# Optimization experiments

Hardware: AMD Instinct MI355X
Metric: run time of the kernel (lower is better)

The kernel has to match this reference:

```python
import jax, jax.numpy as jnp
import numpy as np

B, IN, E, NCLS = 1024, 784, 256, 10
BRAIN, ADIM, NJUMPS = 4, 3, 4
N = BRAIN ** ADIM  # 64 blocks
TAU = 1.0
_GKEY = jax.random.key(42)  # fixed key -> deterministic gumbel noise


def _gumbel_softmax_hard(key, logits):
    u = jax.random.uniform(key, logits.shape, minval=1e-6, maxval=1.0 - 1e-6)
    g = -jnp.log(-jnp.log(u))
    y = jax.nn.softmax((logits + g) / TAU, axis=-1)
    hard = jax.nn.one_hot(jnp.argmax(y, axis=-1), logits.shape[-1], dtype=y.dtype)
    return jax.lax.stop_gradient(hard - y) + y  # straight-through


def _next_address(state, key, at0_W1, at0_b1, at0_W2, at0_b2):
    # always uses block 0's address_transform (as in the original forward)
    h = jax.nn.relu(state @ at0_W1 + at0_b1)
    logits = (h @ at0_W2 + at0_b2).reshape(state.shape[0], ADIM, BRAIN)
    return _gumbel_softmax_hard(key, logits)  # (B, ADIM, BRAIN) one-hot


def _all_blocks(state, st_W1, st_b1, st_W2, st_b2):
    # state: (B,E); st_W*: (N,E,E) stored (in,out). Two batched GEMMs over all N blocks.
    h = jax.nn.relu(jnp.einsum('be,neh->bnh', state, st_W1) + st_b1[None])
    h = jax.nn.relu(jnp.einsum('bnh,nhg->bng', h, st_W2) + st_b2[None])
    norm = jnp.linalg.norm(state, axis=1, keepdims=True)  # (B,1), norm of INPUT state
    return h / (norm[:, :, None] + 1e-6)  # (B,N,E)


def _flatten_onehot(oh):
    # (B, ADIM, BRAIN) -> (B, BRAIN**ADIM) via iterated outer product
    b = oh.shape[0]
    fw = oh[:, 0, :]
    for d in range(1, oh.shape[1]):
        fw = (fw[:, :, None] * oh[:, d, None, :]).reshape(b, -1)
    return fw


def _forward(x, W_emb, b_emb, st_W1, st_b1, st_W2, st_b2,
             at0_W1, at0_b1, at0_W2, at0_b2, out_W1, out_b1, out_W2, out_b2):
    bsz = x.shape[0]
    state = x.reshape(bsz, -1) @ W_emb + b_emb
    initial_state = state
    current_address = _next_address(state, jax.random.fold_in(_GKEY, 0),
                                    at0_W1, at0_b1, at0_W2, at0_b2)
    exited = jnp.zeros((bsz,), dtype=bool)
    exit_states = jnp.zeros_like(state)
    exit_addresses = jnp.zeros_like(current_address)
    for i in range(NJUMPS):  # fixed small jump count; early-break replaced by masking (same math)
        active = ~exited
        bw = _flatten_onehot(current_address)                      # (B,N)
        allout = _all_blocks(state, st_W1, st_b1, st_W2, st_b2)    # (B,N,E)
        new_state = jnp.einsum('bn,bne->be', bw, allout)
        new_address = _next_address(new_state, jax.random.fold_in(_GKEY, i + 1),
                                    at0_W1, at0_b1, at0_W2, at0_b2)
        idx = jnp.argmax(new_address, axis=2)
        is_origin = jnp.all(idx == 0, axis=1) & active
        exit_states = jnp.where(is_origin[:, None], new_state, exit_states)
        exit_addresses = jnp.where(is_origin[:, None, None], new_address, exit_addresses)
        exited = exited | is_origin
        state = jnp.where(active[:, None], new_state, state)
        current_address = jnp.where(active[:, None, None], new_address, current_address)
    final_address = jnp.where(exited[:, None, None], exit_addresses, current_address)
    bw = _flatten_onehot(final_address)
    # original code computes block_out twice and keeps the one using `state` (bug-faithful)
    allout = _all_blocks(state, st_W1, st_b1, st_W2, st_b2)
    final_output = jnp.einsum('bn,bne->be', bw, allout) + initial_state
    h = jax.nn.relu(final_output @ out_W1 + out_b1)
    return h @ out_W2 + out_b2  # (B, NCLS)


def setup_inputs() -> dict:
    key = jax.random.key(0)
    ks = jax.random.split(key, 16)
    s = 0.02
    return {
        'x': jax.random.normal(ks[0], (B, IN), jnp.float32),
        'W_emb': jax.random.normal(ks[1], (IN, E), jnp.float32) * s,
        'b_emb': jnp.zeros((E,), jnp.float32),
        'st_W1': jax.random.normal(ks[2], (N, E, E), jnp.float32) * s,
        'st_b1': jnp.zeros((N, E), jnp.float32),
        'st_W2': jax.random.normal(ks[3], (N, E, E), jnp.float32) * s,
        'st_b2': jnp.zeros((N, E), jnp.float32),
        'at0_W1': jax.random.normal(ks[4], (E, E), jnp.float32) * s,
        'at0_b1': jnp.zeros((E,), jnp.float32),
        'at0_W2': jax.random.normal(ks[5], (E, ADIM * BRAIN), jnp.float32) * s,
        'at0_b2': jnp.zeros((ADIM * BRAIN,), jnp.float32),
        'out_W1': jax.random.normal(ks[6], (E, E), jnp.float32) * s,
        'out_b1': jnp.zeros((E,), jnp.float32),
        'out_W2': jax.random.normal(ks[7], (E, NCLS), jnp.float32) * s,
        'out_b2': jnp.zeros((NCLS,), jnp.float32),
    }


def reference(x, W_emb, b_emb, st_W1, st_b1, st_W2, st_b2,
              at0_W1, at0_b1, at0_W2, at0_b2, out_W1, out_b1, out_W2, out_b2):
    return _forward(x, W_emb, b_emb, st_W1, st_b1, st_W2, st_b2,
                    at0_W1, at0_b1, at0_W2, at0_b2, out_W1, out_b1, out_W2, out_b2)
```

## Files before the change

kernel.cpp:

```cpp
#include <hip/hip_runtime.h>
#include <stdint.h>


#define BATCH 1024
#define EDIM  256
#define INDIM 784
#define CH    4
#define GRID_B 304

__host__ __device__ inline uint32_t rotl32(uint32_t x, uint32_t d) {
  return (x << d) | (x >> (32u - d));
}
__host__ __device__ inline void threefry2x32(uint32_t k0, uint32_t k1,
                                             uint32_t x0, uint32_t x1,
                                             uint32_t* o0, uint32_t* o1) {
  uint32_t ks2 = k0 ^ k1 ^ 0x1BD11BDAu;
  x0 += k0; x1 += k1;
#define TF_R(a) { x0 += x1; x1 = rotl32(x1, a); x1 ^= x0; }
  TF_R(13) TF_R(15) TF_R(26) TF_R(6)   x0 += k1;  x1 += ks2 + 1u;
  TF_R(17) TF_R(29) TF_R(16) TF_R(24)  x0 += ks2; x1 += k0  + 2u;
  TF_R(13) TF_R(15) TF_R(26) TF_R(6)   x0 += k0;  x1 += k1  + 3u;
  TF_R(17) TF_R(29) TF_R(16) TF_R(24)  x0 += k1;  x1 += ks2 + 4u;
  TF_R(13) TF_R(15) TF_R(26) TF_R(6)   x0 += ks2; x1 += k0  + 5u;
#undef TF_R
  *o0 = x0; *o1 = x1;
}
__device__ inline uint32_t jax_bits12288(uint32_t k0, uint32_t k1, uint32_t L) {
  uint32_t o0, o1;
  if (L < 6144u) { threefry2x32(k0, k1, L, L + 6144u, &o0, &o1); return o0; }
  else           { threefry2x32(k0, k1, L - 6144u, L, &o0, &o1); return o1; }
}
__device__ inline float jax_uniform(uint32_t bits) {
  const float minv = 1e-6f;
  const float maxv = (float)(1.0 - 1e-06);
  const float span = maxv - minv;
  uint32_t fb = (bits >> 9) | 0x3f800000u;
  float f = __uint_as_float(fb) - 1.0f;
  float u = __fadd_rn(__fmul_rn(f, span), minv);
  return fmaxf(minv, u);
}
__device__ inline float gumbel_val(int s, int b, int c) {
  uint32_t fk0, fk1;
  threefry2x32(0u, 42u, 0u, (uint32_t)s, &fk0, &fk1);
  const uint32_t L = (uint32_t)(b * 12 + c);
  const float u = jax_uniform(jax_bits12288(fk0, fk1, L));
  return -logf(-logf(u));
}
__device__ inline int addr_argmax(const float* v) {
  int i0 = 0, i1 = 0, i2 = 0;
  { float b = v[0];
    for (int c = 1; c < 4; c++) { float x = v[c];     if (x > b) { b = x; i0 = c; } } }
  { float b = v[4];
    for (int c = 1; c < 4; c++) { float x = v[4 + c]; if (x > b) { b = x; i1 = c; } } }
  { float b = v[8];
    for (int c = 1; c < 4; c++) { float x = v[8 + c]; if (x > b) { b = x; i2 = c; } } }
  return i0 * 16 + i1 * 4 + i2;
}

#define GEMM_TILE(Wbase, XSarr, SROW, kb, KS, acc)                              \
  {                                                                             \
    const float* Wc = (Wbase) + (size_t)(kb) * EDIM + jc;                       \
    _Pragma("unroll 1")                                                         \
    for (int kk = 0; kk < (KS); kk += 4) {                                      \
      float wv[16];                                                             \
      _Pragma("unroll")                                                         \
      for (int q = 0; q < 4; q++) {                                             \
        _Pragma("unroll")                                                       \
        for (int cc = 0; cc < 4; cc++)                                          \
          wv[q * 4 + cc] = Wc[(size_t)(kk + q) * EDIM + cc * 64];               \
      }                                                                         \
      const int k = (kb) + kk;                                                  \
      const float4 r0 = *(const float4*)&(XSarr)[0 * (SROW) + k];               \
      const float4 r1 = *(const float4*)&(XSarr)[1 * (SROW) + k];               \
      const float4 r2 = *(const float4*)&(XSarr)[2 * (SROW) + k];               \
      const float4 r3 = *(const float4*)&(XSarr)[3 * (SROW) + k];               \
      _Pragma("unroll")                                                         \
      for (int cc = 0; cc < 4; cc++) {                                          \
        acc[0][cc] = fmaf(r0.x, wv[0 + cc], acc[0][cc]);                        \
        acc[0][cc] = fmaf(r0.y, wv[4 + cc], acc[0][cc]);                        \
        acc[0][cc] = fmaf(r0.z, wv[8 + cc], acc[0][cc]);                        \
        acc[0][cc] = fmaf(r0.w, wv[12 + cc], acc[0][cc]);                       \
        acc[1][cc] = fmaf(r1.x, wv[0 + cc], acc[1][cc]);                        \
        acc[1][cc] = fmaf(r1.y, wv[4 + cc], acc[1][cc]);                        \
        acc[1][cc] = fmaf(r1.z, wv[8 + cc], acc[1][cc]);                        \
        acc[1][cc] = fmaf(r1.w, wv[12 + cc], acc[1][cc]);                       \
        acc[2][cc] = fmaf(r2.x, wv[0 + cc], acc[2][cc]);                        \
        acc[2][cc] = fmaf(r2.y, wv[4 + cc], acc[2][cc]);                        \
        acc[2][cc] = fmaf(r2.z, wv[8 + cc], acc[2][cc]);                        \
        acc[2][cc] = fmaf(r2.w, wv[12 + cc], acc[2][cc]);                       \
        acc[3][cc] = fmaf(r3.x, wv[0 + cc], acc[3][cc]);                        \
        acc[3][cc] = fmaf(r3.y, wv[4 + cc], acc[3][cc]);                        \
        acc[3][cc] = fmaf(r3.z, wv[8 + cc], acc[3][cc]);                        \
        acc[3][cc] = fmaf(r3.w, wv[12 + cc], acc[3][cc]);                       \
      }                                                                         \
    }                                                                           \
  }

#define P_STORE(P, kg, jc, acc)                                                 \
  { _Pragma("unroll")                                                           \
    for (int cc = 0; cc < 4; cc++) {                                            \
      const int col = (jc) + cc * 64;                                           \
      *(float4*)&(P)[(((kg) * 256) + col) * 4] =                                \
        make_float4(acc[0][cc], acc[1][cc], acc[2][cc], acc[3][cc]);            \
    } }

#define GEMM_TILE_H(Wbase, Harr, kb, KS, acc)                                   \
  {                                                                             \
    const float* Wc = (Wbase) + (size_t)(kb) * EDIM + jc;                       \
    _Pragma("unroll 1")                                                         \
    for (int kk = 0; kk < (KS); kk += 4) {                                      \
      float wv[16];                                                             \
      _Pragma("unroll")                                                         \
      for (int q = 0; q < 4; q++) {                                             \
        _Pragma("unroll")                                                       \
        for (int cc = 0; cc < 4; cc++)                                          \
          wv[q * 4 + cc] = Wc[(size_t)(kk + q) * EDIM + cc * 64];               \
      }                                                                         \
      _Pragma("unroll")                                                         \
      for (int q = 0; q < 4; q++) {                                             \
        const float4 h = *(const float4*)&(Harr)[((kb) + kk + q) * 4];          \
        _Pragma("unroll")                                                       \
        for (int cc = 0; cc < 4; cc++) {                                        \
          acc[0][cc] = fmaf(h.x, wv[q * 4 + cc], acc[0][cc]);                   \
          acc[1][cc] = fmaf(h.y, wv[q * 4 + cc], acc[1][cc]);                   \
          acc[2][cc] = fmaf(h.z, wv[q * 4 + cc], acc[2][cc]);                   \
          acc[3][cc] = fmaf(h.w, wv[q * 4 + cc], acc[3][cc]);                   \
        }                                                                       \
      }                                                                         \
    }                                                                           \
  }

#define ADDR_TAIL(P, H, P2a, vals, ab1, aW2, ab2, astep, b0)                    \
  {                                                                             \
    { const int col = t;                                                        \
      float4 p0 = *(const float4*)&(P)[((0 * 256) + col) * 4];                  \
      float4 p1 = *(const float4*)&(P)[((1 * 256) + col) * 4];                  \
      float4 p2 = *(const float4*)&(P)[((2 * 256) + col) * 4];                  \
      float4 p3 = *(const float4*)&(P)[((3 * 256) + col) * 4];                  \
      const float bb = (ab1)[col];                                              \
      *(float4*)&(H)[col * 4] = make_float4(                                    \
        fmaxf(p0.x + p1.x + p2.x + p3.x + bb, 0.f),                             \
        fmaxf(p0.y + p1.y + p2.y + p3.y + bb, 0.f),                             \
        fmaxf(p0.z + p1.z + p2.z + p3.z + bb, 0.f),                             \
        fmaxf(p0.w + p1.w + p2.w + p3.w + bb, 0.f));                            \
    }                                                                           \
    __syncthreads();                                                            \
    { const int c = t & 15, ksl = t >> 4;                                       \
      float a2[4] = {0.f, 0.f, 0.f, 0.f};                                       \
      if (c < 12) {                                                             \
        const int k0 = ksl * 16;                                                \
        _Pragma("unroll 4")                                                     \
        for (int k = k0; k < k0 + 16; k++) {                                    \
          const float4 h = *(const float4*)&(H)[k * 4];                         \
          const float w = (aW2)[k * 12 + c];                                    \
          a2[0] = fmaf(h.x, w, a2[0]); a2[1] = fmaf(h.y, w, a2[1]);             \
          a2[2] = fmaf(h.z, w, a2[2]); a2[3] = fmaf(h.w, w, a2[3]);             \
        }                                                                       \
      }                                                                         \
      *(float4*)&(P2a)[(ksl * 16 + c) * 4] = make_float4(a2[0], a2[1], a2[2], a2[3]); \
    }                                                                           \
    __syncthreads();                                                            \
    if (t < 48) {                                                               \
      const int i = t / 12, c = t % 12;                                         \
      float s = 0.f;                                                            \
      _Pragma("unroll")                                                         \
      for (int w = 0; w < 16; w++) s += (P2a)[(w * 16 + c) * 4 + i];            \
      (vals)[i * 12 + c] = s + (ab2)[c] + gumbel_val((astep), (b0) + i, c);     \
    }                                                                           \
    __syncthreads();                                                            \
  }

__global__ __launch_bounds__(256, 4) void k_embed_a0(
    const float* __restrict__ x, const float* __restrict__ Wemb,
    const float* __restrict__ bemb,
    const float* __restrict__ aW1, const float* __restrict__ ab1,
    const float* __restrict__ aW2, const float* __restrict__ ab2,
    float* __restrict__ state, float* __restrict__ initial,
    int* __restrict__ nn_all) {
  __shared__ __align__(16) float XS[4 * INDIM];
  __shared__ __align__(16) float P[4 * 256 * 4];
  __shared__ __align__(16) float SS[4 * EDIM];
  __shared__ __align__(16) float H[EDIM * 4];
  __shared__ __align__(16) float P2a[16 * 16 * 4];
  __shared__ float vals[4 * 12];
  const int t = threadIdx.x, b0 = blockIdx.x * 4;
  const int jc = t & 63, kg = t >> 6;

  { const float4* src = (const float4*)(x + (size_t)b0 * INDIM);
    for (int p = t; p < INDIM; p += 256) ((float4*)XS)[p] = src[p];
  }
  __syncthreads();

  {
    const int kb = kg * 196;
    float acc[4][4] = {};
    GEMM_TILE(Wemb, XS, INDIM, kb, 196, acc);
    P_STORE(P, kg, jc, acc);
  }
  __syncthreads();
  {
    const int col = t;
    float4 p0 = *(const float4*)&P[((0 * 256) + col) * 4];
    float4 p1 = *(const float4*)&P[((1 * 256) + col) * 4];
    float4 p2 = *(const float4*)&P[((2 * 256) + col) * 4];
    float4 p3 = *(const float4*)&P[((3 * 256) + col) * 4];
    const float bb = bemb[col];
    float s0 = p0.x + p1.x + p2.x + p3.x + bb;
    float s1 = p0.y + p1.y + p2.y + p3.y + bb;
    float s2 = p0.z + p1.z + p2.z + p3.z + bb;
    float s3 = p0.w + p1.w + p2.w + p3.w + bb;
    SS[0 * EDIM + col] = s0; SS[1 * EDIM + col] = s1;
    SS[2 * EDIM + col] = s2; SS[3 * EDIM + col] = s3;
    state[(size_t)(b0 + 0) * EDIM + col] = s0; initial[(size_t)(b0 + 0) * EDIM + col] = s0;
    state[(size_t)(b0 + 1) * EDIM + col] = s1; initial[(size_t)(b0 + 1) * EDIM + col] = s1;
    state[(size_t)(b0 + 2) * EDIM + col] = s2; initial[(size_t)(b0 + 2) * EDIM + col] = s2;
    state[(size_t)(b0 + 3) * EDIM + col] = s3; initial[(size_t)(b0 + 3) * EDIM + col] = s3;
  }
  __syncthreads();

  {
    const int kb = kg * 64;
    float acc[4][4] = {};
    GEMM_TILE(aW1, SS, EDIM, kb, 64, acc);
    P_STORE(P, kg, jc, acc);
  }
  __syncthreads();
  ADDR_TAIL(P, H, P2a, vals, ab1, aW2, ab2, 0, b0);
  if (t < 4) nn_all[b0 + t] = addr_argmax(&vals[t * 12]);
}

__global__ __launch_bounds__(256, 4) void k_addr(
    const float* __restrict__ state,
    const float* __restrict__ aW1, const float* __restrict__ ab1,
    const float* __restrict__ aW2, const float* __restrict__ ab2,
    const int* __restrict__ nn_prev, int* __restrict__ nn_out, int step) {
  __shared__ __align__(16) float XS[4 * EDIM];
  __shared__ __align__(16) float P[4 * 256 * 4];
  __shared__ __align__(16) float H[EDIM * 4];
  __shared__ __align__(16) float P2a[16 * 16 * 4];
  __shared__ float vals[4 * 12];
  const int t = threadIdx.x, b0 = blockIdx.x * 4;
  const int jc = t & 63, kg = t >> 6;

  ((float4*)XS)[t] = ((const float4*)(state + (size_t)b0 * EDIM))[t];
  __syncthreads();

  { const int kb = kg * 64;
    float acc[4][4] = {};
    GEMM_TILE(aW1, XS, EDIM, kb, 64, acc);
    P_STORE(P, kg, jc, acc);
  }
  __syncthreads();
  ADDR_TAIL(P, H, P2a, vals, ab1, aW2, ab2, step, b0);
  if (t < 4) {
    const int b = b0 + t;
    int nxt;
    if (nn_prev[b] < 0) nxt = -1;
    else {
      const int nn = addr_argmax(&vals[t * 12]);
      nxt = (step < 4 && nn == 0) ? -1 : nn;
    }
    nn_out[b] = nxt;
  }
}

#define B_ROUTE(nnval_expr)                                                     \
  if (t < 64) hist[t] = 0;                                                      \
  if (t < 4) rowsl[t] = 0;                                                      \
  __syncthreads();                                                              \
  int myv[4]; bool fl[4];                                                       \
  _Pragma("unroll")                                                             \
  for (int p = 0; p < 4; p++) {                                                 \
    const int rr = p * 256 + t;                                                 \
    myv[p] = (nnval_expr);                                                      \
    if (myv[p] >= 0) atomicAdd(&hist[myv[p]], 1);                               \
  }                                                                             \
  __syncthreads();                                                              \
  if (t < 64) {                                                                 \
    const int cnt = hist[t];                                                    \
    const int nch = (cnt + CH - 1) / CH;                                        \
    int icnt = cnt, inch = nch;                                                 \
    _Pragma("unroll")                                                           \
    for (int d = 1; d < 64; d <<= 1) {                                          \
      int t1 = __shfl_up(icnt, d), t2 = __shfl_up(inch, d);                     \
      if (t >= d) { icnt += t1; inch += t2; }                                   \
    }                                                                           \
    const int ench = inch - nch;                                                \
    if (t == 63) meta[3] = inch;                                                \
    if (c >= ench && c < ench + nch) {                                          \
      meta[0] = t; meta[1] = c - ench;                                          \
      meta[2] = min(CH, cnt - (c - ench) * CH);                                 \
    }                                                                           \
  }                                                                             \
  __syncthreads();                                                              \
  if (c >= meta[3]) return;                                                     \
  const int n = meta[0], local = meta[1], m = meta[2];                          \
  {                                                                             \
    const int wid = t >> 6, lane = t & 63;                                      \
    unsigned long long bals[4];                                                 \
    _Pragma("unroll")                                                           \
    for (int p = 0; p < 4; p++) {                                               \
      fl[p] = (myv[p] == n);                                                    \
      bals[p] = __ballot(fl[p]);                                                \
      if (lane == 0) wcnt2[p * 4 + wid] = __popcll(bals[p]);                    \
    }                                                                           \
    __syncthreads();                                                            \
    if (t == 0) { int s = 0;                                                    \
      for (int e = 0; e < 16; e++) { wbase2[e] = s; s += wcnt2[e]; } }          \
    __syncthreads();                                                            \
    const int r0 = local * CH;                                                  \
    _Pragma("unroll")                                                           \
    for (int p = 0; p < 4; p++) {                                               \
      if (fl[p]) {                                                              \
        const int rank = wbase2[p * 4 + wid] +                                  \
          __popcll(bals[p] & ((1ull << lane) - 1ull));                          \
        if (rank >= r0 && rank < r0 + CH) rowsl[rank - r0] = p * 256 + t;       \
      }                                                                         \
    }                                                                           \
    __syncthreads();                                                            \
  }

__global__ __launch_bounds__(256, 4) void k_blocks(
    float* __restrict__ state,
    const float* __restrict__ W1, const float* __restrict__ b1,
    const float* __restrict__ W2, const float* __restrict__ b2,
    const int* __restrict__ nnj) {
  __shared__ __align__(16) float XS[4 * EDIM];
  __shared__ __align__(16) float P[4 * 256 * 4];
  __shared__ __align__(16) float H[EDIM * 4];
  __shared__ int hist[64], meta[4], rowsl[4];
  __shared__ int wcnt2[16], wbase2[16];
  __shared__ float denom[4];
  const int t = threadIdx.x;
  const int c = ((blockIdx.x & 7) * 38) + (blockIdx.x >> 3);
  const int jc = t & 63, kg = t >> 6;

  B_ROUTE(nnj[rr])

  {
    const int i = t >> 6, q = t & 63;
    const int row = rowsl[min(i, m - 1)] & 1023;
    const float4 v = *(const float4*)(state + (size_t)row * EDIM + q * 4);
    ((float4*)XS)[t] = v;
    float sq = v.x * v.x + v.y * v.y + v.z * v.z + v.w * v.w;
#pragma unroll
    for (int d = 32; d >= 1; d >>= 1) sq += __shfl_xor(sq, d);
    if (q == 0) denom[i] = sqrtf(sq) + 1e-6f;
  }
  __syncthreads();

  const float* W1n = W1 + (size_t)n * EDIM * EDIM;
  const float* W2n = W2 + (size_t)n * EDIM * EDIM;
  const int kb = kg * 64;
  { float acc[4][4] = {};
    GEMM_TILE(W1n, XS, EDIM, kb, 64, acc);
    P_STORE(P, kg, jc, acc);
  }
  __syncthreads();
  {
    const int col = t;
    float4 p0 = *(const float4*)&P[((0 * 256) + col) * 4];
    float4 p1 = *(const float4*)&P[((1 * 256) + col) * 4];
    float4 p2 = *(const float4*)&P[((2 * 256) + col) * 4];
    float4 p3 = *(const float4*)&P[((3 * 256) + col) * 4];
    const float bb = b1[(size_t)n * EDIM + col];
    *(float4*)&H[col * 4] = make_float4(
      fmaxf(p0.x + p1.x + p2.x + p3.x + bb, 0.f),
      fmaxf(p0.y + p1.y + p2.y + p3.y + bb, 0.f),
      fmaxf(p0.z + p1.z + p2.z + p3.z + bb, 0.f),
      fmaxf(p0.w + p1.w + p2.w + p3.w + bb, 0.f));
  }
  __syncthreads();
  { float acc[4][4] = {};
    GEMM_TILE_H(W2n, H, kb, 64, acc);
    P_STORE(P, kg, jc, acc);
  }
  __syncthreads();
  {
    const int col = t;
    float4 p0 = *(const float4*)&P[((0 * 256) + col) * 4];
    float4 p1 = *(const float4*)&P[((1 * 256) + col) * 4];
    float4 p2 = *(const float4*)&P[((2 * 256) + col) * 4];
    float4 p3 = *(const float4*)&P[((3 * 256) + col) * 4];
    const float bb = b2[(size_t)n * EDIM + col];
    float s[4] = { p0.x + p1.x + p2.x + p3.x + bb,
                   p0.y + p1.y + p2.y + p3.y + bb,
                   p0.z + p1.z + p2.z + p3.z + bb,
                   p0.w + p1.w + p2.w + p3.w + bb };
#pragma unroll
    for (int i = 0; i < 4; i++) {
      if (i < m) {
        const int row = rowsl[i] & 1023;
        state[(size_t)row * EDIM + col] = fmaxf(s[i], 0.f) / denom[i];
      }
    }
  }
}

__global__ __launch_bounds__(256, 4) void k_block_final(
    const float* __restrict__ state,
    const float* __restrict__ W1, const float* __restrict__ b1,
    const float* __restrict__ W2, const float* __restrict__ b2,
    const float* __restrict__ initial,
    const float* __restrict__ oW1, const float* __restrict__ ob1,
    const float* __restrict__ oW2, const float* __restrict__ ob2,
    const int* __restrict__ nn4, float* __restrict__ out) {
  __shared__ __align__(16) float XS[4 * EDIM];
  __shared__ __align__(16) float P[4 * 256 * 4];
  __shared__ __align__(16) float H[EDIM * 4];
  __shared__ __align__(16) float P2h[8 * 16 * 4];
  __shared__ int hist[64], meta[4], rowsl[4];
  __shared__ int wcnt2[16], wbase2[16];
  __shared__ float denom[4];
  const int t = threadIdx.x;
  const int c = ((blockIdx.x & 7) * 38) + (blockIdx.x >> 3);
  const int jc = t & 63, kg = t >> 6;

  B_ROUTE(max(nn4[rr], 0))

  { const int i = t >> 6, q = t & 63;
    const int row = rowsl[min(i, m - 1)] & 1023;
    const float4 v = *(const float4*)(state + (size_t)row * EDIM + q * 4);
    ((float4*)XS)[t] = v;
    float sq = v.x * v.x + v.y * v.y + v.z * v.z + v.w * v.w;
#pragma unroll
    for (int d = 32; d >= 1; d >>= 1) sq += __shfl_xor(sq, d);
    if (q == 0) denom[i] = sqrtf(sq) + 1e-6f;
  }
  __syncthreads();

  const float* W1n = W1 + (size_t)n * EDIM * EDIM;
  const float* W2n = W2 + (size_t)n * EDIM * EDIM;
  const int kb = kg * 64;
  { float acc[4][4] = {};
    GEMM_TILE(W1n, XS, EDIM, kb, 64, acc);
    P_STORE(P, kg, jc, acc);
  }
  __syncthreads();
  { const int col = t;
    float4 p0 = *(const float4*)&P[((0 * 256) + col) * 4];
    float4 p1 = *(const float4*)&P[((1 * 256) + col) * 4];
    float4 p2 = *(const float4*)&P[((2 * 256) + col) * 4];
    float4 p3 = *(const float4*)&P[((3 * 256) + col) * 4];
    const float bb = b1[(size_t)n * EDIM + col];
    *(float4*)&H[col * 4] = make_float4(
      fmaxf(p0.x + p1.x + p2.x + p3.x + bb, 0.f),
      fmaxf(p0.y + p1.y + p2.y + p3.y + bb, 0.f),
      fmaxf(p0.z + p1.z + p2.z + p3.z + bb, 0.f),
      fmaxf(p0.w + p1.w + p2.w + p3.w + bb, 0.f));
  }
  __syncthreads();
  { float acc[4][4] = {};
    GEMM_TILE_H(W2n, H, kb, 64, acc);
    P_STORE(P, kg, jc, acc);
  }
  __syncthreads();
  {
    const int col = t;
    float4 p0 = *(const float4*)&P[((0 * 256) + col) * 4];
    float4 p1 = *(const float4*)&P[((1 * 256) + col) * 4];
    float4 p2 = *(const float4*)&P[((2 * 256) + col) * 4];
    float4 p3 = *(const float4*)&P[((3 * 256) + col) * 4];
    const float bb = b2[(size_t)n * EDIM + col];
    float s[4] = { p0.x + p1.x + p2.x + p3.x + bb,
                   p0.y + p1.y + p2.y + p3.y + bb,
                   p0.z + p1.z + p2.z + p3.z + bb,
                   p0.w + p1.w + p2.w + p3.w + bb };
#pragma unroll
    for (int i = 0; i < 4; i++) {
      const int row = rowsl[i] & 1023;
      float v = fmaxf(s[i], 0.f) / denom[i];
      v += initial[(size_t)row * EDIM + col];
      XS[i * EDIM + col] = v;
    }
  }
  __syncthreads();

  { float acc[4][4] = {};
    GEMM_TILE(oW1, XS, EDIM, kb, 64, acc);
    P_STORE(P, kg, jc, acc);
  }
  __syncthreads();
  { const int col = t;
    float4 p0 = *(const float4*)&P[((0 * 256) + col) * 4];
    float4 p1 = *(const float4*)&P[((1 * 256) + col) * 4];
    float4 p2 = *(const float4*)&P[((2 * 256) + col) * 4];
    float4 p3 = *(const float4*)&P[((3 * 256) + col) * 4];
    const float bb = ob1[col];
    *(float4*)&H[col * 4] = make_float4(
      fmaxf(p0.x + p1.x + p2.x + p3.x + bb, 0.f),
      fmaxf(p0.y + p1.y + p2.y + p3.y + bb, 0.f),
      fmaxf(p0.z + p1.z + p2.z + p3.z + bb, 0.f),
      fmaxf(p0.w + p1.w + p2.w + p3.w + bb, 0.f));
  }
  __syncthreads();
  {
    if (t < 128) {
      const int cc = t & 15, ksl = t >> 4;
      float a2[4] = {0.f, 0.f, 0.f, 0.f};
      if (cc < 10) {
        const int k0 = ksl * 32;
#pragma unroll 4
        for (int k = k0; k < k0 + 32; k++) {
          const float4 h = *(const float4*)&H[k * 4];
          const float w = oW2[k * 10 + cc];
          a2[0] = fmaf(h.x, w, a2[0]); a2[1] = fmaf(h.y, w, a2[1]);
          a2[2] = fmaf(h.z, w, a2[2]); a2[3] = fmaf(h.w, w, a2[3]);
        }
      }
      *(float4*)&P2h[(ksl * 16 + cc) * 4] = make_float4(a2[0], a2[1], a2[2], a2[3]);
    }
  }
  __syncthreads();
  if (t < 40) {
    const int i = t / 10, cc = t % 10;
    if (i < m) {
      float s = 0.f;
#pragma unroll
      for (int w = 0; w < 8; w++) s += P2h[(w * 16 + cc) * 4 + i];
      const int row = rowsl[i] & 1023;
      out[(size_t)row * 10 + cc] = s + ob2[cc];
    }
  }
}

extern "C" void kernel_launch(void* const* d_in, const int* in_sizes, int n_in,
                              void* d_out, int out_size, void* d_ws, size_t ws_size,
                              hipStream_t stream) {
  const float* x    = (const float*)d_in[0];
  const float* Wemb = (const float*)d_in[1];
  const float* bemb = (const float*)d_in[2];
  const float* stW1 = (const float*)d_in[3];
  const float* stb1 = (const float*)d_in[4];
  const float* stW2 = (const float*)d_in[5];
  const float* stb2 = (const float*)d_in[6];
  const float* aW1  = (const float*)d_in[7];
  const float* ab1  = (const float*)d_in[8];
  const float* aW2  = (const float*)d_in[9];
  const float* ab2  = (const float*)d_in[10];
  const float* oW1  = (const float*)d_in[11];
  const float* ob1  = (const float*)d_in[12];
  const float* oW2  = (const float*)d_in[13];
  const float* ob2  = (const float*)d_in[14];
  float* out = (float*)d_out;

  char* ws = (char*)d_ws;
  auto alloc = [&](size_t bytes) { char* p = ws; ws += (bytes + 255) & ~(size_t)255; return p; };
  float* state   = (float*)alloc((size_t)BATCH * EDIM * 4);
  float* initial = (float*)alloc((size_t)BATCH * EDIM * 4);
  int*   nn_all  = (int*)alloc(5 * BATCH * 4);

  k_embed_a0<<<BATCH / 4, 256, 0, stream>>>(x, Wemb, bemb, aW1, ab1, aW2, ab2,
                                            state, initial, nn_all);
  for (int j = 0; j < 4; j++) {
    k_blocks<<<GRID_B, 256, 0, stream>>>(state, stW1, stb1, stW2, stb2,
                                         nn_all + j * BATCH);
    k_addr<<<BATCH / 4, 256, 0, stream>>>(state, aW1, ab1, aW2, ab2,
                                          nn_all + j * BATCH,
                                          nn_all + (j + 1) * BATCH, j + 1);
  }
  k_block_final<<<GRID_B, 256, 0, stream>>>(state, stW1, stb1, stW2, stb2,
                                            initial, oW1, ob1, oW2, ob2,
                                            nn_all + 4 * BATCH, out);
}
```

Baseline: 255.2 us.

## Double thread count per block with 8-way split-K and double-buffered weight loads

All kernels move from 256 to 512 threads, splitting the K dimension of each GEMM tile across 8 thread groups instead of 4, with an 8-way shared-memory partial-sum reduction. The GEMM inner loops now prefetch the next group of weight values into a second register buffer while the current one is used, to hide global load latency. The aim is more warps in flight per block for these latency-bound small GEMMs, at the cost of more shared memory, a longer reduction, and idle threads in the reduction phases.

```diff
diff --git a/kernel.cpp b/kernel.cpp
--- a/kernel.cpp
+++ b/kernel.cpp
@@ -57,100 +57,106 @@
   return i0 * 16 + i1 * 4 + i2;
 }
 
+#define LDW16(dst, Wc, kkq)                                                     \
+  { _Pragma("unroll")                                                           \
+    for (int _q = 0; _q < 4; _q++) {                                            \
+      _Pragma("unroll")                                                         \
+      for (int _cc = 0; _cc < 4; _cc++)                                         \
+        dst[_q * 4 + _cc] = (Wc)[(size_t)((kkq) + _q) * EDIM + _cc * 64];       \
+    } }
+
+#define FMA16(acc, wv, XSarr, SROW, kabs)                                       \
+  { const float4 _r0 = *(const float4*)&(XSarr)[0 * (SROW) + (kabs)];           \
+    const float4 _r1 = *(const float4*)&(XSarr)[1 * (SROW) + (kabs)];           \
+    const float4 _r2 = *(const float4*)&(XSarr)[2 * (SROW) + (kabs)];           \
+    const float4 _r3 = *(const float4*)&(XSarr)[3 * (SROW) + (kabs)];           \
+    _Pragma("unroll")                                                           \
+    for (int _cc = 0; _cc < 4; _cc++) {                                         \
+      acc[0][_cc] = fmaf(_r0.x, wv[0 + _cc], acc[0][_cc]);                      \
+      acc[0][_cc] = fmaf(_r0.y, wv[4 + _cc], acc[0][_cc]);                      \
+      acc[0][_cc] = fmaf(_r0.z, wv[8 + _cc], acc[0][_cc]);                      \
+      acc[0][_cc] = fmaf(_r0.w, wv[12 + _cc], acc[0][_cc]);                     \
+      acc[1][_cc] = fmaf(_r1.x, wv[0 + _cc], acc[1][_cc]);                      \
+      acc[1][_cc] = fmaf(_r1.y, wv[4 + _cc], acc[1][_cc]);                      \
+      acc[1][_cc] = fmaf(_r1.z, wv[8 + _cc], acc[1][_cc]);                      \
+      acc[1][_cc] = fmaf(_r1.w, wv[12 + _cc], acc[1][_cc]);                     \
+      acc[2][_cc] = fmaf(_r2.x, wv[0 + _cc], acc[2][_cc]);                      \
+      acc[2][_cc] = fmaf(_r2.y, wv[4 + _cc], acc[2][_cc]);                      \
+      acc[2][_cc] = fmaf(_r2.z, wv[8 + _cc], acc[2][_cc]);                      \
+      acc[2][_cc] = fmaf(_r2.w, wv[12 + _cc], acc[2][_cc]);                     \
+      acc[3][_cc] = fmaf(_r3.x, wv[0 + _cc], acc[3][_cc]);                      \
+      acc[3][_cc] = fmaf(_r3.y, wv[4 + _cc], acc[3][_cc]);                      \
+      acc[3][_cc] = fmaf(_r3.z, wv[8 + _cc], acc[3][_cc]);                      \
+      acc[3][_cc] = fmaf(_r3.w, wv[12 + _cc], acc[3][_cc]);                     \
+    } }
+
 #define GEMM_TILE(Wbase, XSarr, SROW, kb, KS, acc)                              \
-  {                                                                             \
-    const float* Wc = (Wbase) + (size_t)(kb) * EDIM + jc;                       \
+  { const float* _Wc = (Wbase) + (size_t)(kb) * EDIM + jc;                      \
+    float _wvA[16], _wvB[16];                                                   \
+    LDW16(_wvA, _Wc, 0)                                                         \
     _Pragma("unroll 1")                                                         \
-    for (int kk = 0; kk < (KS); kk += 4) {                                      \
-      float wv[16];                                                             \
+    for (int _kk = 0; _kk < (KS); _kk += 8) {                                   \
+      LDW16(_wvB, _Wc, _kk + 4)                                                 \
+      FMA16(acc, _wvA, XSarr, SROW, (kb) + _kk)                                 \
+      if (_kk + 8 < (KS)) LDW16(_wvA, _Wc, _kk + 8)                             \
+      FMA16(acc, _wvB, XSarr, SROW, (kb) + _kk + 4)                             \
+    } }
+
+#define FMA16H(acc, wv, Harr, kabs)                                             \
+  { _Pragma("unroll")                                                           \
+    for (int _q = 0; _q < 4; _q++) {                                            \
+      const float4 _h = *(const float4*)&(Harr)[((kabs) + _q) * 4];             \
       _Pragma("unroll")                                                         \
-      for (int q = 0; q < 4; q++) {                                             \
-        _Pragma("unroll")                                                       \
-        for (int cc = 0; cc < 4; cc++)                                          \
-          wv[q * 4 + cc] = Wc[(size_t)(kk + q) * EDIM + cc * 64];               \
-      }                                                                         \
-      const int k = (kb) + kk;                                                  \
-      const float4 r0 = *(const float4*)&(XSarr)[0 * (SROW) + k];               \
-      const float4 r1 = *(const float4*)&(XSarr)[1 * (SROW) + k];               \
-      const float4 r2 = *(const float4*)&(XSarr)[2 * (SROW) + k];               \
-      const float4 r3 = *(const float4*)&(XSarr)[3 * (SROW) + k];               \
-      _Pragma("unroll")                                                         \
-      for (int cc = 0; cc < 4; cc++) {                                          \
-        acc[0][cc] = fmaf(r0.x, wv[0 + cc], acc[0][cc]);                        \
-        acc[0][cc] = fmaf(r0.y, wv[4 + cc], acc[0][cc]);                        \
-        acc[0][cc] = fmaf(r0.z, wv[8 + cc], acc[0][cc]);                        \
-        acc[0][cc] = fmaf(r0.w, wv[12 + cc], acc[0][cc]);                       \
-        acc[1][cc] = fmaf(r1.x, wv[0 + cc], acc[1][cc]);                        \
-        acc[1][cc] = fmaf(r1.y, wv[4 + cc], acc[1][cc]);                        \
-        acc[1][cc] = fmaf(r1.z, wv[8 + cc], acc[1][cc]);                        \
-        acc[1][cc] = fmaf(r1.w, wv[12 + cc], acc[1][cc]);                       \
-        acc[2][cc] = fmaf(r2.x, wv[0 + cc], acc[2][cc]);                        \
-        acc[2][cc] = fmaf(r2.y, wv[4 + cc], acc[2][cc]);                        \
-        acc[2][cc] = fmaf(r2.z, wv[8 + cc], acc[2][cc]);                        \
-        acc[2][cc] = fmaf(r2.w, wv[12 + cc], acc[2][cc]);                       \
-        acc[3][cc] = fmaf(r3.x, wv[0 + cc], acc[3][cc]);                        \
-        acc[3][cc] = fmaf(r3.y, wv[4 + cc], acc[3][cc]);                        \
-        acc[3][cc] = fmaf(r3.z, wv[8 + cc], acc[3][cc]);                        \
-        acc[3][cc] = fmaf(r3.w, wv[12 + cc], acc[3][cc]);                       \
-      }                                                                         \
-    }                                                                           \
-  }
+      for (int _cc = 0; _cc < 4; _cc++) {                                       \
+        acc[0][_cc] = fmaf(_h.x, wv[_q * 4 + _cc], acc[0][_cc]);                \
+        acc[1][_cc] = fmaf(_h.y, wv[_q * 4 + _cc], acc[1][_cc]);                \
+        acc[2][_cc] = fmaf(_h.z, wv[_q * 4 + _cc], acc[2][_cc]);                \
+        acc[3][_cc] = fmaf(_h.w, wv[_q * 4 + _cc], acc[3][_cc]);                \
+      } } }
+
+#define GEMM_TILE_H(Wbase, Harr, kb, KS, acc)                                   \
+  { const float* _Wc = (Wbase) + (size_t)(kb) * EDIM + jc;                      \
+    float _wvA[16], _wvB[16];                                                   \
+    LDW16(_wvA, _Wc, 0)                                                         \
+    _Pragma("unroll 1")                                                         \
+    for (int _kk = 0; _kk < (KS); _kk += 8) {                                   \
+      LDW16(_wvB, _Wc, _kk + 4)                                                 \
+      FMA16H(acc, _wvA, Harr, (kb) + _kk)                                       \
+      if (_kk + 8 < (KS)) LDW16(_wvA, _Wc, _kk + 8)                             \
+      FMA16H(acc, _wvB, Harr, (kb) + _kk + 4)                                   \
+    } }
 
 #define P_STORE(P, kg, jc, acc)                                                 \
   { _Pragma("unroll")                                                           \
-    for (int cc = 0; cc < 4; cc++) {                                            \
-      const int col = (jc) + cc * 64;                                           \
-      *(float4*)&(P)[(((kg) * 256) + col) * 4] =                                \
-        make_float4(acc[0][cc], acc[1][cc], acc[2][cc], acc[3][cc]);            \
+    for (int _cc = 0; _cc < 4; _cc++) {                                         \
+      const int _col = (jc) + _cc * 64;                                         \
+      *(float4*)&(P)[(((kg) * 256) + _col) * 4] =                               \
+        make_float4(acc[0][_cc], acc[1][_cc], acc[2][_cc], acc[3][_cc]);        \
     } }
 
-#define GEMM_TILE_H(Wbase, Harr, kb, KS, acc)                                   \
-  {                                                                             \
-    const float* Wc = (Wbase) + (size_t)(kb) * EDIM + jc;                       \
-    _Pragma("unroll 1")                                                         \
-    for (int kk = 0; kk < (KS); kk += 4) {                                      \
-      float wv[16];                                                             \
-      _Pragma("unroll")                                                         \
-      for (int q = 0; q < 4; q++) {                                             \
-        _Pragma("unroll")                                                       \
-        for (int cc = 0; cc < 4; cc++)                                          \
-          wv[q * 4 + cc] = Wc[(size_t)(kk + q) * EDIM + cc * 64];               \
-      }                                                                         \
-      _Pragma("unroll")                                                         \
-      for (int q = 0; q < 4; q++) {                                             \
-        const float4 h = *(const float4*)&(Harr)[((kb) + kk + q) * 4];          \
-        _Pragma("unroll")                                                       \
-        for (int cc = 0; cc < 4; cc++) {                                        \
-          acc[0][cc] = fmaf(h.x, wv[q * 4 + cc], acc[0][cc]);                   \
-          acc[1][cc] = fmaf(h.y, wv[q * 4 + cc], acc[1][cc]);                   \
-          acc[2][cc] = fmaf(h.z, wv[q * 4 + cc], acc[2][cc]);                   \
-          acc[3][cc] = fmaf(h.w, wv[q * 4 + cc], acc[3][cc]);                   \
-        }                                                                       \
-      }                                                                         \
-    }                                                                           \
-  }
+#define P_REDUCE8(P, col, bias, dst4)                                           \
+  { float4 _ps = *(const float4*)&(P)[(col) * 4];                               \
+    _Pragma("unroll")                                                           \
+    for (int _pw = 1; _pw < 8; _pw++) {                                         \
+      const float4 _pp = *(const float4*)&(P)[((_pw * 256) + (col)) * 4];       \
+      _ps.x += _pp.x; _ps.y += _pp.y; _ps.z += _pp.z; _ps.w += _pp.w;           \
+    }                                                                           \
+    _ps.x += (bias); _ps.y += (bias); _ps.z += (bias); _ps.w += (bias);         \
+    dst4 = _ps; }
 
 #define ADDR_TAIL(P, H, P2a, vals, ab1, aW2, ab2, astep, b0)                    \
-  {                                                                             \
-    { const int col = t;                                                        \
-      float4 p0 = *(const float4*)&(P)[((0 * 256) + col) * 4];                  \
-      float4 p1 = *(const float4*)&(P)[((1 * 256) + col) * 4];                  \
-      float4 p2 = *(const float4*)&(P)[((2 * 256) + col) * 4];                  \
-      float4 p3 = *(const float4*)&(P)[((3 * 256) + col) * 4];                  \
-      const float bb = (ab1)[col];                                              \
-      *(float4*)&(H)[col * 4] = make_float4(                                    \
-        fmaxf(p0.x + p1.x + p2.x + p3.x + bb, 0.f),                             \
-        fmaxf(p0.y + p1.y + p2.y + p3.y + bb, 0.f),                             \
-        fmaxf(p0.z + p1.z + p2.z + p3.z + bb, 0.f),                             \
-        fmaxf(p0.w + p1.w + p2.w + p3.w + bb, 0.f));                            \
+  { if (t < 256) {                                                              \
+      float4 s; P_REDUCE8(P, t, (ab1)[t], s);                                   \
+      *(float4*)&(H)[t * 4] = make_float4(fmaxf(s.x, 0.f), fmaxf(s.y, 0.f),     \
+                                          fmaxf(s.z, 0.f), fmaxf(s.w, 0.f));    \
     }                                                                           \
     __syncthreads();                                                            \
     { const int c = t & 15, ksl = t >> 4;                                       \
       float a2[4] = {0.f, 0.f, 0.f, 0.f};                                       \
       if (c < 12) {                                                             \
-        const int k0 = ksl * 16;                                                \
-        _Pragma("unroll 4")                                                     \
-        for (int k = k0; k < k0 + 16; k++) {                                    \
+        const int k0 = ksl * 8;                                                 \
+        _Pragma("unroll")                                                       \
+        for (int k = k0; k < k0 + 8; k++) {                                     \
           const float4 h = *(const float4*)&(H)[k * 4];                         \
           const float w = (aW2)[k * 12 + c];                                    \
           a2[0] = fmaf(h.x, w, a2[0]); a2[1] = fmaf(h.y, w, a2[1]);             \
@@ -164,13 +170,13 @@
       const int i = t / 12, c = t % 12;                                         \
       float s = 0.f;                                                            \
       _Pragma("unroll")                                                         \
-      for (int w = 0; w < 16; w++) s += (P2a)[(w * 16 + c) * 4 + i];            \
+      for (int w = 0; w < 32; w++) s += (P2a)[(w * 16 + c) * 4 + i];            \
       (vals)[i * 12 + c] = s + (ab2)[c] + gumbel_val((astep), (b0) + i, c);     \
     }                                                                           \
     __syncthreads();                                                            \
   }
 
-__global__ __launch_bounds__(256, 4) void k_embed_a0(
+__global__ __launch_bounds__(512, 2) void k_embed_a0(
     const float* __restrict__ x, const float* __restrict__ Wemb,
     const float* __restrict__ bemb,
     const float* __restrict__ aW1, const float* __restrict__ ab1,
@@ -178,50 +184,42 @@
     float* __restrict__ state, float* __restrict__ initial,
     int* __restrict__ nn_all) {
   __shared__ __align__(16) float XS[4 * INDIM];
-  __shared__ __align__(16) float P[4 * 256 * 4];
+  __shared__ __align__(16) float P[8 * 256 * 4];
   __shared__ __align__(16) float SS[4 * EDIM];
   __shared__ __align__(16) float H[EDIM * 4];
-  __shared__ __align__(16) float P2a[16 * 16 * 4];
+  __shared__ __align__(16) float P2a[32 * 16 * 4];
   __shared__ float vals[4 * 12];
   const int t = threadIdx.x, b0 = blockIdx.x * 4;
   const int jc = t & 63, kg = t >> 6;
 
   { const float4* src = (const float4*)(x + (size_t)b0 * INDIM);
-    for (int p = t; p < INDIM; p += 256) ((float4*)XS)[p] = src[p];
+    for (int p = t; p < INDIM; p += 512) ((float4*)XS)[p] = src[p];
   }
   __syncthreads();
 
   {
-    const int kb = kg * 196;
+    const int kb = (kg < 2) ? kg * 104 : 208 + (kg - 2) * 96;
     float acc[4][4] = {};
-    GEMM_TILE(Wemb, XS, INDIM, kb, 196, acc);
-    P_STORE(P, kg, jc, acc);
-  }
-  __syncthreads();
+    if (kg < 2) { GEMM_TILE(Wemb, XS, INDIM, kb, 104, acc); }
+    else        { GEMM_TILE(Wemb, XS, INDIM, kb, 96, acc); }
+    P_STORE(P, kg, jc, acc);
+  }
+  __syncthreads();
+  if (t < 256) {
+    float4 s; P_REDUCE8(P, t, bemb[t], s);
+    SS[0 * EDIM + t] = s.x; SS[1 * EDIM + t] = s.y;
+    SS[2 * EDIM + t] = s.z; SS[3 * EDIM + t] = s.w;
+    state[(size_t)(b0 + 0) * EDIM + t] = s.x; initial[(size_t)(b0 + 0) * EDIM + t] = s.x;
+    state[(size_t)(b0 + 1) * EDIM + t] = s.y; initial[(size_t)(b0 + 1) * EDIM + t] = s.y;
+    state[(size_t)(b0 + 2) * EDIM + t] = s.z; initial[(size_t)(b0 + 2) * EDIM + t] = s.z;
+    state[(size_t)(b0 + 3) * EDIM + t] = s.w; initial[(size_t)(b0 + 3) * EDIM + t] = s.w;
+  }
+  __syncthreads();
+
   {
-    const int col = t;
-    float4 p0 = *(const float4*)&P[((0 * 256) + col) * 4];
-    float4 p1 = *(const float4*)&P[((1 * 256) + col) * 4];
-    float4 p2 = *(const float4*)&P[((2 * 256) + col) * 4];
-    float4 p3 = *(const float4*)&P[((3 * 256) + col) * 4];
-    const float bb = bemb[col];
-    float s0 = p0.x + p1.x + p2.x + p3.x + bb;
-    float s1 = p0.y + p1.y + p2.y + p3.y + bb;
-    float s2 = p0.z + p1.z + p2.z + p3.z + bb;
-    float s3 = p0.w + p1.w + p2.w + p3.w + bb;
-    SS[0 * EDIM + col] = s0; SS[1 * EDIM + col] = s1;
-    SS[2 * EDIM + col] = s2; SS[3 * EDIM + col] = s3;
-    state[(size_t)(b0 + 0) * EDIM + col] = s0; initial[(size_t)(b0 + 0) * EDIM + col] = s0;
-    state[(size_t)(b0 + 1) * EDIM + col] = s1; initial[(size_t)(b0 + 1) * EDIM + col] = s1;
-    state[(size_t)(b0 + 2) * EDIM + col] = s2; initial[(size_t)(b0 + 2) * EDIM + col] = s2;
-    state[(size_t)(b0 + 3) * EDIM + col] = s3; initial[(size_t)(b0 + 3) * EDIM + col] = s3;
-  }
-  __syncthreads();
-
-  {
-    const int kb = kg * 64;
+    const int kb = kg * 32;
     float acc[4][4] = {};
-    GEMM_TILE(aW1, SS, EDIM, kb, 64, acc);
+    GEMM_TILE(aW1, SS, EDIM, kb, 32, acc);
     P_STORE(P, kg, jc, acc);
   }
   __syncthreads();
@@ -229,25 +227,25 @@
   if (t < 4) nn_all[b0 + t] = addr_argmax(&vals[t * 12]);
 }
 
-__global__ __launch_bounds__(256, 4) void k_addr(
+__global__ __launch_bounds__(512, 2) void k_addr(
     const float* __restrict__ state,
     const float* __restrict__ aW1, const float* __restrict__ ab1,
     const float* __restrict__ aW2, const float* __restrict__ ab2,
     const int* __restrict__ nn_prev, int* __restrict__ nn_out, int step) {
   __shared__ __align__(16) float XS[4 * EDIM];
-  __shared__ __align__(16) float P[4 * 256 * 4];
+  __shared__ __align__(16) float P[8 * 256 * 4];
   __shared__ __align__(16) float H[EDIM * 4];
-  __shared__ __align__(16) float P2a[16 * 16 * 4];
+  __shared__ __align__(16) float P2a[32 * 16 * 4];
   __shared__ float vals[4 * 12];
   const int t = threadIdx.x, b0 = blockIdx.x * 4;
   const int jc = t & 63, kg = t >> 6;
 
-  ((float4*)XS)[t] = ((const float4*)(state + (size_t)b0 * EDIM))[t];
-  __syncthreads();
-
-  { const int kb = kg * 64;
+  if (t < 256) ((float4*)XS)[t] = ((const float4*)(state + (size_t)b0 * EDIM))[t];
+  __syncthreads();
+
+  { const int kb = kg * 32;
     float acc[4][4] = {};
-    GEMM_TILE(aW1, XS, EDIM, kb, 64, acc);
+    GEMM_TILE(aW1, XS, EDIM, kb, 32, acc);
     P_STORE(P, kg, jc, acc);
   }
   __syncthreads();
@@ -268,10 +266,10 @@
   if (t < 64) hist[t] = 0;                                                      \
   if (t < 4) rowsl[t] = 0;                                                      \
   __syncthreads();                                                              \
-  int myv[4]; bool fl[4];                                                       \
+  int myv[2]; bool fl[2];                                                       \
   _Pragma("unroll")                                                             \
-  for (int p = 0; p < 4; p++) {                                                 \
-    const int rr = p * 256 + t;                                                 \
+  for (int p = 0; p < 2; p++) {                                                 \
+    const int rr = p * 512 + t;                                                 \
     myv[p] = (nnval_expr);                                                      \
     if (myv[p] >= 0) atomicAdd(&hist[myv[p]], 1);                               \
   }                                                                             \
@@ -297,12 +295,12 @@
   const int n = meta[0], local = meta[1], m = meta[2];                          \
   {                                                                             \
     const int wid = t >> 6, lane = t & 63;                                      \
-    unsigned long long bals[4];                                                 \
+    unsigned long long bals[2];                                                 \
     _Pragma("unroll")                                                           \
-    for (int p = 0; p < 4; p++) {                                               \
+    for (int p = 0; p < 2; p++) {                                               \
       fl[p] = (myv[p] == n);                                                    \
       bals[p] = __ballot(fl[p]);                                                \
-      if (lane == 0) wcnt2[p * 4 + wid] = __popcll(bals[p]);                    \
+      if (lane == 0) wcnt2[p * 8 + wid] = __popcll(bals[p]);                    \
     }                                                                           \
     __syncthreads();                                                            \
     if (t == 0) { int s = 0;                                                    \
@@ -310,23 +308,23 @@
     __syncthreads();                                                            \
     const int r0 = local * CH;                                                  \
     _Pragma("unroll")                                                           \
-    for (int p = 0; p < 4; p++) {                                               \
+    for (int p = 0; p < 2; p++) {                                               \
       if (fl[p]) {                                                              \
-        const int rank = wbase2[p * 4 + wid] +                                  \
+        const int rank = wbase2[p * 8 + wid] +                                  \
           __popcll(bals[p] & ((1ull << lane) - 1ull));                          \
-        if (rank >= r0 && rank < r0 + CH) rowsl[rank - r0] = p * 256 + t;       \
+        if (rank >= r0 && rank < r0 + CH) rowsl[rank - r0] = p * 512 + t;       \
       }                                                                         \
     }                                                                           \
     __syncthreads();                                                            \
   }
 
-__global__ __launch_bounds__(256, 4) void k_blocks(
+__global__ __launch_bounds__(512, 2) void k_blocks(
     float* __restrict__ state,
     const float* __restrict__ W1, const float* __restrict__ b1,
     const float* __restrict__ W2, const float* __restrict__ b2,
     const int* __restrict__ nnj) {
   __shared__ __align__(16) float XS[4 * EDIM];
-  __shared__ __align__(16) float P[4 * 256 * 4];
+  __shared__ __align__(16) float P[8 * 256 * 4];
   __shared__ __align__(16) float H[EDIM * 4];
   __shared__ int hist[64], meta[4], rowsl[4];
   __shared__ int wcnt2[16], wbase2[16];
@@ -337,7 +335,7 @@
 
   B_ROUTE(nnj[rr])
 
-  {
+  if (t < 256) {
     const int i = t >> 6, q = t & 63;
     const int row = rowsl[min(i, m - 1)] & 1023;
     const float4 v = *(const float4*)(state + (size_t)row * EDIM + q * 4);
@@ -351,53 +349,37 @@
 
   const float* W1n = W1 + (size_t)n * EDIM * EDIM;
   const float* W2n = W2 + (size_t)n * EDIM * EDIM;
-  const int kb = kg * 64;
+  const int kb = kg * 32;
   { float acc[4][4] = {};
-    GEMM_TILE(W1n, XS, EDIM, kb, 64, acc);
-    P_STORE(P, kg, jc, acc);
-  }
-  __syncthreads();
-  {
-    const int col = t;
-    float4 p0 = *(const float4*)&P[((0 * 256) + col) * 4];
-    float4 p1 = *(const float4*)&P[((1 * 256) + col) * 4];
-    float4 p2 = *(const float4*)&P[((2 * 256) + col) * 4];
-    float4 p3 = *(const float4*)&P[((3 * 256) + col) * 4];
-    const float bb = b1[(size_t)n * EDIM + col];
-    *(float4*)&H[col * 4] = make_float4(
-      fmaxf(p0.x + p1.x + p2.x + p3.x + bb, 0.f),
-      fmaxf(p0.y + p1.y + p2.y + p3.y + bb, 0.f),
-      fmaxf(p0.z + p1.z + p2.z + p3.z + bb, 0.f),
-      fmaxf(p0.w + p1.w + p2.w + p3.w + bb, 0.f));
+    GEMM_TILE(W1n, XS, EDIM, kb, 32, acc);
+    P_STORE(P, kg, jc, acc);
+  }
+  __syncthreads();
+  if (t < 256) {
+    float4 s; P_REDUCE8(P, t, b1[(size_t)n * EDIM + t], s);
+    *(float4*)&H[t * 4] = make_float4(fmaxf(s.x, 0.f), fmaxf(s.y, 0.f),
+                                      fmaxf(s.z, 0.f), fmaxf(s.w, 0.f));
   }
   __syncthreads();
   { float acc[4][4] = {};
-    GEMM_TILE_H(W2n, H, kb, 64, acc);
-    P_STORE(P, kg, jc, acc);
-  }
-  __syncthreads();
-  {
-    const int col = t;
-    float4 p0 = *(const float4*)&P[((0 * 256) + col) * 4];
-    float4 p1 = *(const float4*)&P[((1 * 256) + col) * 4];
-    float4 p2 = *(const float4*)&P[((2 * 256) + col) * 4];
-    float4 p3 = *(const float4*)&P[((3 * 256) + col) * 4];
-    const float bb = b2[(size_t)n * EDIM + col];
-    float s[4] = { p0.x + p1.x + p2.x + p3.x + bb,
-                   p0.y + p1.y + p2.y + p3.y + bb,
-                   p0.z + p1.z + p2.z + p3.z + bb,
-                   p0.w + p1.w + p2.w + p3.w + bb };
+    GEMM_TILE_H(W2n, H, kb, 32, acc);
+    P_STORE(P, kg, jc, acc);
+  }
+  __syncthreads();
+  if (t < 256) {
+    float4 s; P_REDUCE8(P, t, b2[(size_t)n * EDIM + t], s);
+    float sv[4] = { s.x, s.y, s.z, s.w };
 #pragma unroll
     for (int i = 0; i < 4; i++) {
       if (i < m) {
         const int row = rowsl[i] & 1023;
-        state[(size_t)row * EDIM + col] = fmaxf(s[i], 0.f) / denom[i];
+        state[(size_t)row * EDIM + t] = fmaxf(sv[i], 0.f) / denom[i];
       }
     }
   }
 }
 
-__global__ __launch_bounds__(256, 4) void k_block_final(
+__global__ __launch_bounds__(512, 2) void k_block_final(
     const float* __restrict__ state,
     const float* __restrict__ W1, const float* __restrict__ b1,
     const float* __restrict__ W2, const float* __restrict__ b2,
@@ -406,9 +388,9 @@
     const float* __restrict__ oW2, const float* __restrict__ ob2,
     const int* __restrict__ nn4, float* __restrict__ out) {
   __shared__ __align__(16) float XS[4 * EDIM];
-  __shared__ __align__(16) float P[4 * 256 * 4];
+  __shared__ __align__(16) float P[8 * 256 * 4];
   __shared__ __align__(16) float H[EDIM * 4];
-  __shared__ __align__(16) float P2h[8 * 16 * 4];
+  __shared__ __align__(16) float P2h[32 * 16 * 4];
   __shared__ int hist[64], meta[4], rowsl[4];
   __shared__ int wcnt2[16], wbase2[16];
   __shared__ float denom[4];
@@ -418,7 +400,8 @@
 
   B_ROUTE(max(nn4[rr], 0))
 
-  { const int i = t >> 6, q = t & 63;
+  if (t < 256) {
+    const int i = t >> 6, q = t & 63;
     const int row = rowsl[min(i, m - 1)] & 1023;
     const float4 v = *(const float4*)(state + (size_t)row * EDIM + q * 4);
     ((float4*)XS)[t] = v;
@@ -431,85 +414,61 @@
 
   const float* W1n = W1 + (size_t)n * EDIM * EDIM;
   const float* W2n = W2 + (size_t)n * EDIM * EDIM;
-  const int kb = kg * 64;
+  const int kb = kg * 32;
   { float acc[4][4] = {};
-    GEMM_TILE(W1n, XS, EDIM, kb, 64, acc);
-    P_STORE(P, kg, jc, acc);
-  }
-  __syncthreads();
-  { const int col = t;
-    float4 p0 = *(const float4*)&P[((0 * 256) + col) * 4];
-    float4 p1 = *(const float4*)&P[((1 * 256) + col) * 4];
-    float4 p2 = *(const float4*)&P[((2 * 256) + col) * 4];
-    float4 p3 = *(const float4*)&P[((3 * 256) + col) * 4];
-    const float bb = b1[(size_t)n * EDIM + col];
-    *(float4*)&H[col * 4] = make_float4(
-      fmaxf(p0.x + p1.x + p2.x + p3.x + bb, 0.f),
-      fmaxf(p0.y + p1.y + p2.y + p3.y + bb, 0.f),
-      fmaxf(p0.z + p1.z + p2.z + p3.z + bb, 0.f),
-      fmaxf(p0.w + p1.w + p2.w + p3.w + bb, 0.f));
+    GEMM_TILE(W1n, XS, EDIM, kb, 32, acc);
+    P_STORE(P, kg, jc, acc);
+  }
+  __syncthreads();
+  if (t < 256) {
+    float4 s; P_REDUCE8(P, t, b1[(size_t)n * EDIM + t], s);
+    *(float4*)&H[t * 4] = make_float4(fmaxf(s.x, 0.f), fmaxf(s.y, 0.f),
+                                      fmaxf(s.z, 0.f), fmaxf(s.w, 0.f));
   }
   __syncthreads();
   { float acc[4][4] = {};
-    GEMM_TILE_H(W2n, H, kb, 64, acc);
-    P_STORE(P, kg, jc, acc);
-  }
-  __syncthreads();
-  {
-    const int col = t;
-    float4 p0 = *(const float4*)&P[((0 * 256) + col) * 4];
-    float4 p1 = *(const float4*)&P[((1 * 256) + col) * 4];
-    float4 p2 = *(const float4*)&P[((2 * 256) + col) * 4];
-    float4 p3 = *(const float4*)&P[((3 * 256) + col) * 4];
-    const float bb = b2[(size_t)n * EDIM + col];
-    float s[4] = { p0.x + p1.x + p2.x + p3.x + bb,
-                   p0.y + p1.y + p2.y + p3.y + bb,
-                   p0.z + p1.z + p2.z + p3.z + bb,
-                   p0.w + p1.w + p2.w + p3.w + bb };
+    GEMM_TILE_H(W2n, H, kb, 32, acc);
+    P_STORE(P, kg, jc, acc);
+  }
+  __syncthreads();
+  if (t < 256) {
+    float4 s; P_REDUCE8(P, t, b2[(size_t)n * EDIM + t], s);
+    float sv[4] = { s.x, s.y, s.z, s.w };
 #pragma unroll
     for (int i = 0; i < 4; i++) {
       const int row = rowsl[i] & 1023;
-      float v = fmaxf(s[i], 0.f) / denom[i];
-      v += initial[(size_t)row * EDIM + col];
-      XS[i * EDIM + col] = v;
+      float v = fmaxf(sv[i], 0.f) / denom[i];
+      v += initial[(size_t)row * EDIM + t];
+      XS[i * EDIM + t] = v;
     }
   }
   __syncthreads();
 
   { float acc[4][4] = {};
-    GEMM_TILE(oW1, XS, EDIM, kb, 64, acc);
-    P_STORE(P, kg, jc, acc);
-  }
-  __syncthreads();
-  { const int col = t;
-    float4 p0 = *(const float4*)&P[((0 * 256) + col) * 4];
-    float4 p1 = *(const float4*)&P[((1 * 256) + col) * 4];
-    float4 p2 = *(const float4*)&P[((2 * 256) + col) * 4];
-    float4 p3 = *(const float4*)&P[((3 * 256) + col) * 4];
-    const float bb = ob1[col];
-    *(float4*)&H[col * 4] = make_float4(
-      fmaxf(p0.x + p1.x + p2.x + p3.x + bb, 0.f),
-      fmaxf(p0.y + p1.y + p2.y + p3.y + bb, 0.f),
-      fmaxf(p0.z + p1.z + p2.z + p3.z + bb, 0.f),
-      fmaxf(p0.w + p1.w + p2.w + p3.w + bb, 0.f));
+    GEMM_TILE(oW1, XS, EDIM, kb, 32, acc);
+    P_STORE(P, kg, jc, acc);
+  }
+  __syncthreads();
+  if (t < 256) {
+    float4 s; P_REDUCE8(P, t, ob1[t], s);
+    *(float4*)&H[t * 4] = make_float4(fmaxf(s.x, 0.f), fmaxf(s.y, 0.f),
+                                      fmaxf(s.z, 0.f), fmaxf(s.w, 0.f));
   }
   __syncthreads();
   {
-    if (t < 128) {
-      const int cc = t & 15, ksl = t >> 4;
-      float a2[4] = {0.f, 0.f, 0.f, 0.f};
-      if (cc < 10) {
-        const int k0 = ksl * 32;
-#pragma unroll 4
-        for (int k = k0; k < k0 + 32; k++) {
-          const float4 h = *(const float4*)&H[k * 4];
-          const float w = oW2[k * 10 + cc];
-          a2[0] = fmaf(h.x, w, a2[0]); a2[1] = fmaf(h.y, w, a2[1]);
-          a2[2] = fmaf(h.z, w, a2[2]); a2[3] = fmaf(h.w, w, a2[3]);
-        }
+    const int cc = t & 15, ksl = t >> 4;
+    float a2[4] = {0.f, 0.f, 0.f, 0.f};
+    if (cc < 10) {
+      const int k0 = ksl * 8;
+#pragma unroll
+      for (int k = k0; k < k0 + 8; k++) {
+        const float4 h = *(const float4*)&H[k * 4];
+        const float w = oW2[k * 10 + cc];
+        a2[0] = fmaf(h.x, w, a2[0]); a2[1] = fmaf(h.y, w, a2[1]);
+        a2[2] = fmaf(h.z, w, a2[2]); a2[3] = fmaf(h.w, w, a2[3]);
       }
-      *(float4*)&P2h[(ksl * 16 + cc) * 4] = make_float4(a2[0], a2[1], a2[2], a2[3]);
     }
+    *(float4*)&P2h[(ksl * 16 + cc) * 4] = make_float4(a2[0], a2[1], a2[2], a2[3]);
   }
   __syncthreads();
   if (t < 40) {
@@ -517,7 +476,7 @@
     if (i < m) {
       float s = 0.f;
 #pragma unroll
-      for (int w = 0; w < 8; w++) s += P2h[(w * 16 + cc) * 4 + i];
+      for (int w = 0; w < 32; w++) s += P2h[(w * 16 + cc) * 4 + i];
       const int row = rowsl[i] & 1023;
       out[(size_t)row * 10 + cc] = s + ob2[cc];
     }
@@ -550,16 +509,16 @@
   float* initial = (float*)alloc((size_t)BATCH * EDIM * 4);
   int*   nn_all  = (int*)alloc(5 * BATCH * 4);
 
-  k_embed_a0<<<BATCH / 4, 256, 0, stream>>>(x, Wemb, bemb, aW1, ab1, aW2, ab2,
+  k_embed_a0<<<BATCH / 4, 512, 0, stream>>>(x, Wemb, bemb, aW1, ab1, aW2, ab2,
                                             state, initial, nn_all);
   for (int j = 0; j < 4; j++) {
-    k_blocks<<<GRID_B, 256, 0, stream>>>(state, stW1, stb1, stW2, stb2,
+    k_blocks<<<GRID_B, 512, 0, stream>>>(state, stW1, stb1, stW2, stb2,
                                          nn_all + j * BATCH);
-    k_addr<<<BATCH / 4, 256, 0, stream>>>(state, aW1, ab1, aW2, ab2,
+    k_addr<<<BATCH / 4, 512, 0, stream>>>(state, aW1, ab1, aW2, ab2,
                                           nn_all + j * BATCH,
                                           nn_all + (j + 1) * BATCH, j + 1);
   }
-  k_block_final<<<GRID_B, 256, 0, stream>>>(state, stW1, stb1, stW2, stb2,
+  k_block_final<<<GRID_B, 512, 0, stream>>>(state, stW1, stb1, stW2, stb2,
                                             initial, oW1, ob1, oW2, ob2,
                                             nn_all + 4 * BATCH, out);
 }
```

Measured after the change: 227.3 us. 10.9% less time.
